# Performance work log

Hardware: AMD Instinct MI355X
Metric: run time of the kernel (lower is better)

The kernel has to match this reference:

```python
import jax, jax.numpy as jnp
import numpy as np
from jax import lax

# dims
B, T_MEL, N_MEL, L_TXT, D_TXT = 8, 400, 80, 128, 512
E, HID, EMB, N_SPK = 256, 256, 128, 100
H = HID // 2  # per-direction LSTM hidden


def setup_inputs() -> dict:
    key = jax.random.key(0)
    ks = jax.random.split(key, 16)
    def n(k, shape, s=0.02):
        return jax.random.normal(k, shape, jnp.float32) * s
    return {
        "x": n(ks[0], (B, N_MEL, T_MEL), 1.0),
        "input_lengths": jax.random.randint(ks[1], (B,), T_MEL // 2, T_MEL + 1).astype(jnp.int32),
        "text": n(ks[2], (B, L_TXT, D_TXT), 1.0),
        "text_lengths": jax.random.randint(ks[3], (B,), L_TXT // 2, L_TXT + 1).astype(jnp.int32),
        "Wx": n(ks[4], (E, N_MEL)), "bx": jnp.zeros((E,), jnp.float32),
        "Wq": n(ks[5], (E, D_TXT)), "bq": jnp.zeros((E,), jnp.float32),
        "Wout": n(ks[6], (E, E)), "bout": jnp.zeros((E,), jnp.float32),
        "v": jax.random.normal(ks[7], (E, 1), jnp.float32) * 0.1,
        "lstm_wih": n(ks[8], (2, 2, 4 * H, HID)),
        "lstm_whh": n(ks[9], (2, 2, 4 * H, H)),
        "lstm_bih": jnp.zeros((2, 2, 4 * H), jnp.float32),
        "lstm_bhh": jnp.zeros((2, 2, 4 * H), jnp.float32),
        "p1_w": n(ks[10], (EMB, HID)), "p1_b": jnp.zeros((EMB,), jnp.float32),
        "p2_w": n(ks[11], (N_SPK, EMB)), "p2_b": jnp.zeros((N_SPK,), jnp.float32),
    }


def _run_lstm(x, Wih, Whh, bih, bhh):
    # x: [B, L, in] -> outputs [B, L, H]; PyTorch gate order i,f,g,o
    h0 = jnp.zeros((x.shape[0], Whh.shape[1]), x.dtype)
    c0 = jnp.zeros_like(h0)
    def step(carry, xt):
        h, c = carry
        g = xt @ Wih.T + h @ Whh.T + (bih + bhh)
        i, f, gg, o = jnp.split(g, 4, axis=-1)
        c = jax.nn.sigmoid(f) * c + jax.nn.sigmoid(i) * jnp.tanh(gg)
        h = jax.nn.sigmoid(o) * jnp.tanh(c)
        return (h, c), h
    _, hs = lax.scan(step, (h0, c0), x.swapaxes(0, 1))  # scan over time
    return hs.swapaxes(0, 1)


def _reverse_by_length(x, lengths):
    # reverse the first lengths[b] steps of each sequence (pack_padded semantics)
    L = x.shape[1]
    idx = jnp.clip(lengths[:, None] - 1 - jnp.arange(L)[None, :], 0, L - 1)
    return jnp.take_along_axis(x, idx[:, :, None], axis=1)


def reference(x, input_lengths, text, text_lengths, Wx, bx, Wq, bq, Wout, bout, v,
              lstm_wih, lstm_whh, lstm_bih, lstm_bhh, p1_w, p1_b, p2_w, p2_b):
    # ---- vectorized VanillaAttention over all text tokens ----
    mels = x.swapaxes(1, 2)                       # [B, T, M]
    x1 = mels @ Wx.T + bx                         # [B, T, E]   linear_x
    q1 = text @ Wq.T + bq                         # [B, L, E]   linear_q
    # v^T @ out_linear(tanh(.)) == tanh(.) @ (Wout^T v) + v . bout
    w = Wout.T @ v[:, 0]                          # [E]
    c = bout @ v[:, 0]                            # scalar
    s = jnp.tanh(x1[:, None, :, :] + q1[:, :, None, :])   # [B, L, T, E]
    scores = jnp.einsum('blte,e->blt', s, w) + c           # [B, L, T]
    mel_mask = jnp.arange(T_MEL)[None, :] < input_lengths[:, None]   # [B, T]
    scores = jnp.where(mel_mask[:, None, :], scores, -jnp.inf)
    scores = jax.nn.softmax(scores, axis=-1)
    contexts = jnp.einsum('blt,bte->ble', scores, x1)       # [B, L, E]
    h = q1 + contexts                                       # LSTM input

    # ---- 2-layer bidirectional LSTM (packed semantics via per-length reversal) ----
    for layer in range(2):
        fwd = _run_lstm(h, lstm_wih[layer, 0], lstm_whh[layer, 0], lstm_bih[layer, 0], lstm_bhh[layer, 0])
        rev = _reverse_by_length(h, text_lengths)
        bwd = _run_lstm(rev, lstm_wih[layer, 1], lstm_whh[layer, 1], lstm_bih[layer, 1], lstm_bhh[layer, 1])
        bwd = _reverse_by_length(bwd, text_lengths)
        h = jnp.concatenate([fwd, bwd], axis=-1)            # [B, L, HID]

    # ---- masked mean pool (pad_packed zeros the padding before the sum) ----
    txt_mask = (jnp.arange(L_TXT)[None, :] < text_lengths[:, None]).astype(h.dtype)
    pooled = (h * txt_mask[:, :, None]).sum(axis=1) / text_lengths[:, None].astype(h.dtype)

    out = jnp.tanh(pooled @ p1_w.T + p1_b)
    embeddings = out / jnp.linalg.norm(out, axis=1, keepdims=True)
    logits = out @ p2_w.T + p2_b
    return logits, embeddings, scores
```

## Files before the change

kernel.cpp:

```cpp
#include <hip/hip_runtime.h>
#include <hip/hip_bf16.h>
#include <math.h>

#define B 8
#define T_MEL 400
#define N_MEL 80
#define L_TXT 128
#define D_TXT 512
#define E 256
#define HID 256
#define EMB 128
#define N_SPK 100
#define HH 128

#define OFF_W      0
#define OFF_C      256
#define OFF_WXT    272
#define OFF_WQT    (OFF_WXT + N_MEL*E)
#define OFF_WIHT   (OFF_WQT + D_TXT*E)
#define OFF_BSUM   (OFF_WIHT + 2*2*256*512)
#define OFF_X1     (OFF_BSUM + 2048)
#define OFF_Q1     (OFF_X1 + B*T_MEL*E)
#define OFF_G      OFF_X1
#define OFF_H0     (OFF_Q1 + B*L_TXT*E)
#define OFF_O1     (OFF_H0 + B*L_TXT*E)
#define OFF_HS0    OFF_H0
#define OFF_HS1    OFF_O1

typedef _Float16 half2v __attribute__((ext_vector_type(2)));

__device__ __forceinline__ float fast_sigmoid(float x){ return 1.f/(1.f+__expf(-x)); }
__device__ __forceinline__ float fast_tanh(float x){ float e=__expf(2.f*x); return 1.f - 2.f/(e+1.f); }

__device__ __forceinline__ float fdot2(uint a, uint b, float c){
  half2v ha = __builtin_bit_cast(half2v, a);
  half2v hb = __builtin_bit_cast(half2v, b);
#if __has_builtin(__builtin_amdgcn_fdot2)
  return __builtin_amdgcn_fdot2(ha, hb, c, false);
#else
  float r;
  asm("v_dot2_f32_f16 %0, %1, %2, %3" : "=v"(r) : "v"(a), "v"(b), "v"(c));
  return r;
#endif
}
__device__ __forceinline__ uint packh2(float a, float b){
  union { _Float16 h[2]; uint u; } x;
  x.h[0] = (_Float16)a; x.h[1] = (_Float16)b; return x.u;
}

__global__ __launch_bounds__(256) void k_prep(const float* __restrict__ Wout, const float* __restrict__ bout,
                       const float* __restrict__ v,    const float* __restrict__ Wx,
                       const float* __restrict__ Wq,   const float* __restrict__ wih,
                       const float* __restrict__ bih,  const float* __restrict__ bhh,
                       float* __restrict__ ws){
  int blk = blockIdx.x, tid = threadIdx.x;
  if (blk == 0){
    float acc = 0.f;
    for (int j=0;j<E;j++) acc += Wout[j*E + tid] * v[j];
    ws[OFF_W + tid] = acc;
    if (tid==0){ float c=0.f; for(int j=0;j<E;j++) c += bout[j]*v[j]; ws[OFF_C]=c; }
  } else if (blk <= N_MEL){
    int m = blk-1;
    ws[OFF_WXT + m*E + tid] = Wx[tid*N_MEL + m];
  } else if (blk <= N_MEL + D_TXT){
    int k = blk-1-N_MEL;
    ws[OFF_WQT + k*E + tid] = Wq[tid*D_TXT + k];
  } else if (blk <= N_MEL + D_TXT + 512){
    int idx = blk-1-N_MEL-D_TXT;
    int ld = idx >> 7, k2 = idx & 127;
    uint* wout = (uint*)(ws + OFF_WIHT) + (size_t)idx*512;
    for (int g = tid; g < 512; g += 256){
      float a = wih[((size_t)(ld*512+g))*256 + 2*k2];
      float b = wih[((size_t)(ld*512+g))*256 + 2*k2 + 1];
      wout[g] = packh2(a, b);
    }
  } else {
    for (int i = tid; i < 2048; i += 256)
      ws[OFF_BSUM + i] = bih[i] + bhh[i];
  }
}

__global__ __launch_bounds__(256) void k_xq(const float* __restrict__ x,    const float* __restrict__ bx,
                                            const float* __restrict__ text, const float* __restrict__ bq,
                                            float* __restrict__ ws){
  __shared__ float sbuf[2048];
  int blk = blockIdx.x, tid = threadIdx.x;
  if (blk < 800){
    int b = blk/100; int t0 = (blk%100)*4;
    float (*sx)[4] = (float(*)[4])sbuf;
    for (int i = tid; i < N_MEL*4; i += 256){
      int m = i>>2, ii = i&3;
      sx[m][ii] = x[(b*N_MEL+m)*T_MEL + t0 + ii];
    }
    __syncthreads();
    float bxe = bx[tid];
    float a0=bxe,a1=bxe,a2=bxe,a3=bxe;
    const float* wxt = ws + OFF_WXT;
    #pragma unroll 4
    for (int m=0;m<N_MEL;m++){
      float w = wxt[m*E + tid];
      a0 += sx[m][0]*w; a1 += sx[m][1]*w; a2 += sx[m][2]*w; a3 += sx[m][3]*w;
    }
    float* x1 = ws + OFF_X1 + (b*T_MEL + t0)*E + tid;
    x1[0]=a0; x1[E]=a1; x1[2*E]=a2; x1[3*E]=a3;
  } else {
    int bb = blk - 800;
    int b = bb/32; int l0 = (bb%32)*4;
    float (*st)[D_TXT] = (float(*)[D_TXT])sbuf;
    for (int i = tid; i < 4*D_TXT; i += 256){
      int li = i / D_TXT, k = i % D_TXT;
      st[li][k] = text[(b*L_TXT + l0 + li)*D_TXT + k];
    }
    __syncthreads();
    float bqe = bq[tid];
    float a0=bqe,a1=bqe,a2=bqe,a3=bqe;
    const float* wqt = ws + OFF_WQT;
    #pragma unroll 2
    for (int k=0;k<D_TXT;k++){
      float w = wqt[k*E + tid];
      a0 += st[0][k]*w; a1 += st[1][k]*w; a2 += st[2][k]*w; a3 += st[3][k]*w;
    }
    float* q1 = ws + OFF_Q1 + (b*L_TXT + l0)*E + tid;
    q1[0]=a0; q1[E]=a1; q1[2*E]=a2; q1[3*E]=a3;
  }
}

__global__ __launch_bounds__(256) void k_score(const int* __restrict__ mel_len,
                                               float* __restrict__ ws,
                                               float* __restrict__ d_out){
  int blk = blockIdx.x; int b = blk >> 7; int l = blk & 127;
  int tid = threadIdx.x; int lane = tid & 63; int wv = tid >> 6;
  __shared__ __align__(16) float sl[T_MEL];
  __shared__ float red[8];
  const float* x1 = ws + OFF_X1 + b*T_MEL*E;
  const float* q1 = ws + OFF_Q1 + (b*L_TXT+l)*E;
  int g = lane >> 4, i = lane & 15;
  float qv[16], wvv[16];
  {
    const float4* q4 = (const float4*)(q1 + i*16);
    const float4* w4 = (const float4*)(ws + OFF_W + i*16);
    #pragma unroll
    for (int j=0;j<4;j++){
      float4 a = q4[j]; qv[4*j]=a.x; qv[4*j+1]=a.y; qv[4*j+2]=a.z; qv[4*j+3]=a.w;
      float4 c = w4[j]; wvv[4*j]=c.x; wvv[4*j+1]=c.y; wvv[4*j+2]=c.z; wvv[4*j+3]=c.w;
    }
  }
  float cc = ws[OFF_C];
  int len = mel_len[b];
  #pragma unroll 2
  for (int iter=0; iter<25; iter++){
    int t = iter*16 + wv*4 + g;
    const float4* xr = (const float4*)(x1 + t*E + i*16);
    float s = 0.f;
    #pragma unroll
    for (int j=0;j<4;j++){
      float4 xv = xr[j];
      s += wvv[4*j+0]*fast_tanh(xv.x + qv[4*j+0]);
      s += wvv[4*j+1]*fast_tanh(xv.y + qv[4*j+1]);
      s += wvv[4*j+2]*fast_tanh(xv.z + qv[4*j+2]);
      s += wvv[4*j+3]*fast_tanh(xv.w + qv[4*j+3]);
    }
    s += __shfl_xor(s,1); s += __shfl_xor(s,2);
    s += __shfl_xor(s,4); s += __shfl_xor(s,8);
    if (i==0) sl[t] = s + cc;
  }
  __syncthreads();
  float mx = -3.0e38f;
  for (int t = tid; t < T_MEL; t += 256) if (t < len) mx = fmaxf(mx, sl[t]);
  #pragma unroll
  for (int off=32; off>=1; off>>=1) mx = fmaxf(mx, __shfl_xor(mx, off));
  if (lane==0) red[wv] = mx;
  __syncthreads();
  mx = fmaxf(fmaxf(red[0],red[1]),fmaxf(red[2],red[3]));
  float se = 0.f;
  for (int t = tid; t < T_MEL; t += 256){
    float p = (t < len) ? __expf(sl[t]-mx) : 0.f;
    sl[t] = p; se += p;
  }
  #pragma unroll
  for (int off=32; off>=1; off>>=1) se += __shfl_xor(se, off);
  if (lane==0) red[4+wv] = se;
  __syncthreads();
  float rsum = 1.f/(red[4]+red[5]+red[6]+red[7]);
  float* sc_out = d_out + 1824 + (b*L_TXT + l)*T_MEL;
  for (int t = tid; t < T_MEL; t += 256){
    float p = sl[t]*rsum;
    sl[t] = p; sc_out[t] = p;
  }
  __syncthreads();
  float a = 0.f;
  int e = tid;
  for (int t = 0; t < T_MEL; t += 4){
    float4 p4 = *(const float4*)&sl[t];
    a += p4.x*x1[(t  )*E+e] + p4.y*x1[(t+1)*E+e]
       + p4.z*x1[(t+2)*E+e] + p4.w*x1[(t+3)*E+e];
  }
  ws[OFF_H0 + (b*L_TXT+l)*E + e] = q1[e] + a;
}

__global__ __launch_bounds__(512) void k_gates(const float* __restrict__ in,
                                               const float* __restrict__ hs,
                                               const int* __restrict__ txt_len,
                                               float* __restrict__ gates, int layer,
                                               float* __restrict__ ws){
  int idx = blockIdx.x; int tt = idx & 15; int dir = (idx>>4)&1; int b = idx>>5;
  int tid = threadIdx.x;
  __shared__ __align__(16) uint sih[8][128];
  int len = txt_len[b];
  for (int i = tid; i < 8*128; i += 512){
    int r = i >> 7, k2 = i & 127;
    int t = tt*8 + r;
    int row = dir ? max(0, len-1-t) : t;
    float va, vb;
    if (layer == 0){
      const float2 p = *(const float2*)&in[((size_t)(b*L_TXT + row))*HID + 2*k2];
      va = p.x; vb = p.y;
    } else {
      int k = 2*k2; int d = k >> 7, u = k & 127;
      int sidx = (d==0) ? row : (row < len ? len-1-row : 0);
      const float* hr = hs + (((size_t)(d*8+b)*128) + u)*128 + sidx;
      va = hr[0]; vb = hr[128];
    }
    sih[r][k2] = packh2(va, vb);
  }
  __syncthreads();
  int ld = layer*2 + dir;
  int g = tid;
  float bsum = ws[OFF_BSUM + ld*512 + g];
  float acc[8];
  #pragma unroll
  for (int r=0;r<8;r++) acc[r] = bsum;
  const uint* wt2 = (const uint*)(ws + OFF_WIHT) + (size_t)ld*128*512 + g;
  for (int k4=0; k4<128; k4+=4){
    uint w0 = wt2[(k4  )*512];
    uint w1 = wt2[(k4+1)*512];
    uint w2 = wt2[(k4+2)*512];
    uint w3 = wt2[(k4+3)*512];
    #pragma unroll
    for (int r=0;r<8;r++){
      uint4 s4 = *(const uint4*)&sih[r][k4];
      acc[r] = fdot2(s4.x, w0, acc[r]);
      acc[r] = fdot2(s4.y, w1, acc[r]);
      acc[r] = fdot2(s4.z, w2, acc[r]);
      acc[r] = fdot2(s4.w, w3, acc[r]);
    }
  }
  float* go = gates + (((size_t)(dir*L_TXT + tt*8)*8) + b)*512 + g;
  #pragma unroll
  for (int r=0;r<8;r++) go[(size_t)r*8*512] = acc[r];
}

__global__ __launch_bounds__(512) void k_scan(const float* __restrict__ Gp,
                                              const float* __restrict__ whh_all,
                                              float* __restrict__ hseq, int layer){
  int dir = blockIdx.x & 1; int b = blockIdx.x >> 1;
  int tid = threadIdx.x;
  int l = tid & 63, w = tid >> 6;
  int gt = l >> 4;
  int li = l & 15;
  int u  = w*16 + li;
  int row = gt*128 + u;

  __shared__ uint wlds[32768];
  __shared__ uint h2buf[2][64];

  const float* wr = whh_all + ((size_t)((layer*2+dir)*512 + row))*HH;
  #pragma unroll
  for (int j=0;j<16;j++){
    uint4 vv;
    vv.x = packh2(wr[j*8+0], wr[j*8+1]);
    vv.y = packh2(wr[j*8+2], wr[j*8+3]);
    vv.z = packh2(wr[j*8+4], wr[j*8+5]);
    vv.w = packh2(wr[j*8+6], wr[j*8+7]);
    *(uint4*)(wlds + w*4096 + j*256 + l*4) = vv;
  }
  if (tid < 128) ((uint*)h2buf)[tid] = 0;

  const float* gb = Gp + ((size_t)(dir*L_TXT)*8 + b)*512 + row;
  float gi = gb[0];
  float c_reg = 0.f;
  float hm1=0.f, hm2=0.f, hm3=0.f;
  bool isg = (gt==2);
  __syncthreads();

  const uint4* wp = (const uint4*)(wlds + w*4096 + l*4);
  float* hout = hseq + (((size_t)(dir*8+b)*128) + u)*128;

  for (int s=0; s<L_TXT; s++){
    float gnext = gb[(size_t)(s+1 < L_TXT ? s+1 : s)*4096];
    const uint4* hp = (const uint4*)(h2buf[s&1]);
    float p0 = gi, p1 = 0.f, p2 = 0.f, p3 = 0.f;
    #pragma unroll
    for (int j=0;j<16;j+=4){
      uint4 A0 = wp[(j  )*64], H0 = hp[j  ];
      uint4 A1 = wp[(j+1)*64], H1 = hp[j+1];
      uint4 A2 = wp[(j+2)*64], H2 = hp[j+2];
      uint4 A3 = wp[(j+3)*64], H3 = hp[j+3];
      p0 = fdot2(A0.x,H0.x,p0); p0 = fdot2(A0.y,H0.y,p0);
      p0 = fdot2(A0.z,H0.z,p0); p0 = fdot2(A0.w,H0.w,p0);
      p1 = fdot2(A1.x,H1.x,p1); p1 = fdot2(A1.y,H1.y,p1);
      p1 = fdot2(A1.z,H1.z,p1); p1 = fdot2(A1.w,H1.w,p1);
      p2 = fdot2(A2.x,H2.x,p2); p2 = fdot2(A2.y,H2.y,p2);
      p2 = fdot2(A2.z,H2.z,p2); p2 = fdot2(A2.w,H2.w,p2);
      p3 = fdot2(A3.x,H3.x,p3); p3 = fdot2(A3.y,H3.y,p3);
      p3 = fdot2(A3.z,H3.z,p3); p3 = fdot2(A3.w,H3.w,p3);
    }
    float acc = (p0+p1)+(p2+p3);
    float xa = isg ? 2.f*acc : acc;
    float sg = 1.f/(1.f+__expf(-xa));
    float val = isg ? 2.f*sg - 1.f : sg;
    float x  = __shfl_xor(val, 16);
    float y0 = __shfl_xor(val, 32);
    float y1 = __shfl_xor(x,   32);
    float iv = (gt==0)?val : (gt==1)?x  : (gt==2)?y0 : y1;
    float fv = (gt==0)?x   : (gt==1)?val: (gt==2)?y1 : y0;
    float gv = (gt==0)?y0  : (gt==1)?y1 : (gt==2)?val: x;
    float ov = (gt==0)?y1  : (gt==1)?y0 : (gt==2)?x  : val;
    c_reg = fv*c_reg + iv*gv;
    float h = ov*fast_tanh(c_reg);
    float hn = __shfl_xor(h, 1);
    if (gt==0 && !(li&1)) h2buf[(s+1)&1][u>>1] = packh2(h, hn);
    if (gt==0 && (s&3)==3)
      *(float4*)&hout[s-3] = make_float4(hm3, hm2, hm1, h);
    hm3 = hm2; hm2 = hm1; hm1 = h;
    gi = gnext;
    __syncthreads();
  }
}

__global__ __launch_bounds__(256) void k_final(const float* __restrict__ hs,
                                               const int* __restrict__ txt_len,
                                               const float* __restrict__ p1w,
                                               const float* __restrict__ p1b,
                                               const float* __restrict__ p2w,
                                               const float* __restrict__ p2b,
                                               float* __restrict__ d_out){
  int b = blockIdx.x; int tid = threadIdx.x;
  __shared__ float pl[HID];
  __shared__ float ol[EMB];
  __shared__ float nrm;
  int len = txt_len[b];
  int d = tid >> 7, u = tid & 127;
  const float* hrow = hs + (((size_t)(d*8+b)*128) + u)*128;
  float s = 0.f;
  int t4 = len & ~3;
  for (int t=0; t<t4; t+=4){
    float4 p = *(const float4*)&hrow[t];
    s += (p.x + p.y) + (p.z + p.w);
  }
  for (int t=t4; t<len; t++) s += hrow[t];
  pl[tid] = s / (float)len;
  __syncthreads();
  if (tid < EMB){
    float a = p1b[tid];
    for (int k=0;k<HID;k++) a += pl[k]*p1w[tid*HID+k];
    ol[tid] = fast_tanh(a);
  }
  __syncthreads();
  if (tid == 0){
    float q = 0.f;
    for (int k=0;k<EMB;k++) q += ol[k]*ol[k];
    nrm = rsqrtf(q);
  }
  __syncthreads();
  if (tid < EMB) d_out[800 + b*EMB + tid] = ol[tid]*nrm;
  if (tid < N_SPK){
    float a = p2b[tid];
    for (int k=0;k<EMB;k++) a += ol[k]*p2w[tid*EMB+k];
    d_out[b*N_SPK + tid] = a;
  }
}

extern "C" void kernel_launch(void* const* d_in, const int* in_sizes, int n_in,
                              void* d_out, int out_size, void* d_ws, size_t ws_size,
                              hipStream_t stream) {
  const float* x       = (const float*)d_in[0];
  const int*   mel_len = (const int*)  d_in[1];
  const float* text    = (const float*)d_in[2];
  const int*   txt_len = (const int*)  d_in[3];
  const float* Wx      = (const float*)d_in[4];
  const float* bx      = (const float*)d_in[5];
  const float* Wq      = (const float*)d_in[6];
  const float* bq      = (const float*)d_in[7];
  const float* Wout    = (const float*)d_in[8];
  const float* bout    = (const float*)d_in[9];
  const float* v       = (const float*)d_in[10];
  const float* wih     = (const float*)d_in[11];
  const float* whh     = (const float*)d_in[12];
  const float* bih     = (const float*)d_in[13];
  const float* bhh     = (const float*)d_in[14];
  const float* p1w     = (const float*)d_in[15];
  const float* p1b     = (const float*)d_in[16];
  const float* p2w     = (const float*)d_in[17];
  const float* p2b     = (const float*)d_in[18];
  float* ws  = (float*)d_ws;
  float* out = (float*)d_out;

  k_prep <<<1106, 256, 0, stream>>>(Wout, bout, v, Wx, Wq, wih, bih, bhh, ws);
  k_xq   <<<1056, 256, 0, stream>>>(x, bx, text, bq, ws);
  k_score<<<1024, 256, 0, stream>>>(mel_len, ws, out);

  float* G = ws + OFF_G;
  k_gates<<<256, 512, 0, stream>>>(ws + OFF_H0, ws + OFF_HS0, txt_len, G, 0, ws);
  k_scan <<<16, 512, 0, stream>>>(G, whh, ws + OFF_HS0, 0);
  k_gates<<<256, 512, 0, stream>>>(ws + OFF_H0, ws + OFF_HS0, txt_len, G, 1, ws);
  k_scan <<<16, 512, 0, stream>>>(G, whh, ws + OFF_HS1, 1);

  k_final<<<8, 256, 0, stream>>>(ws + OFF_HS1, txt_len, p1w, p1b, p2w, p2b, out);
}
```

Baseline: 461.0 us.

## Restructure LSTM scan to compute all four gates per thread pair and fuse pooling

The recurrent scan kernel drops from 512 to 256 threads per block. Each pair of threads now splits the hidden-dimension dot product for all four gates of one unit and combines the halves with a shuffle, replacing the old scheme of one gate per thread with cross-lane gate exchange. In layer 1 the scan accumulates the masked sum for mean pooling directly instead of writing the hidden sequence, so the final kernel reads pooled sums rather than re-reading the full sequence. The aim is less per-step shuffle and select overhead and less sequence traffic, at the cost of more dot-product work per thread on the serial critical path.

```diff
diff --git a/kernel.cpp b/kernel.cpp
--- a/kernel.cpp
+++ b/kernel.cpp
@@ -25,7 +25,7 @@
 #define OFF_H0     (OFF_Q1 + B*L_TXT*E)
 #define OFF_O1     (OFF_H0 + B*L_TXT*E)
 #define OFF_HS0    OFF_H0
-#define OFF_HS1    OFF_O1
+#define OFF_POOL   OFF_O1
 
 typedef _Float16 half2v __attribute__((ext_vector_type(2)));
 
@@ -250,85 +250,97 @@
   for (int r=0;r<8;r++) go[(size_t)r*8*512] = acc[r];
 }
 
-__global__ __launch_bounds__(512) void k_scan(const float* __restrict__ Gp,
+__global__ __launch_bounds__(256) void k_scan(const float* __restrict__ Gp,
                                               const float* __restrict__ whh_all,
-                                              float* __restrict__ hseq, int layer){
+                                              const int* __restrict__ txt_len,
+                                              float* __restrict__ hseq,
+                                              float* __restrict__ pooled, int layer){
   int dir = blockIdx.x & 1; int b = blockIdx.x >> 1;
   int tid = threadIdx.x;
   int l = tid & 63, w = tid >> 6;
-  int gt = l >> 4;
-  int li = l & 15;
-  int u  = w*16 + li;
-  int row = gt*128 + u;
+  int u  = tid >> 1;
+  int hf = tid & 1;
 
   __shared__ uint wlds[32768];
   __shared__ uint h2buf[2][64];
 
-  const float* wr = whh_all + ((size_t)((layer*2+dir)*512 + row))*HH;
+  const float* wbase = whh_all + (size_t)(layer*2+dir)*512*HH;
   #pragma unroll
-  for (int j=0;j<16;j++){
-    uint4 vv;
-    vv.x = packh2(wr[j*8+0], wr[j*8+1]);
-    vv.y = packh2(wr[j*8+2], wr[j*8+3]);
-    vv.z = packh2(wr[j*8+4], wr[j*8+5]);
-    vv.w = packh2(wr[j*8+6], wr[j*8+7]);
-    *(uint4*)(wlds + w*4096 + j*256 + l*4) = vv;
+  for (int r=0;r<4;r++){
+    const float* wr = wbase + (size_t)(r*128+u)*HH + 64*hf;
+    #pragma unroll
+    for (int jj=0;jj<8;jj++){
+      uint4 vv;
+      vv.x = packh2(wr[jj*8+0], wr[jj*8+1]);
+      vv.y = packh2(wr[jj*8+2], wr[jj*8+3]);
+      vv.z = packh2(wr[jj*8+4], wr[jj*8+5]);
+      vv.w = packh2(wr[jj*8+6], wr[jj*8+7]);
+      *(uint4*)(wlds + w*8192 + (r*8+jj)*256 + l*4) = vv;
+    }
   }
   if (tid < 128) ((uint*)h2buf)[tid] = 0;
-
-  const float* gb = Gp + ((size_t)(dir*L_TXT)*8 + b)*512 + row;
-  float gi = gb[0];
-  float c_reg = 0.f;
+  int len = txt_len[b];
+  bool pool = (layer == 1);
+
+  const float* gb = Gp + ((size_t)(dir*L_TXT)*8 + b)*512 + u;
+  float g0 = gb[0], g1 = gb[128], g2 = gb[256], g3 = gb[384];
+  float c_reg = 0.f, psum = 0.f;
   float hm1=0.f, hm2=0.f, hm3=0.f;
-  bool isg = (gt==2);
-  __syncthreads();
-
-  const uint4* wp = (const uint4*)(wlds + w*4096 + l*4);
+  __syncthreads();
+
+  const uint4* wp = (const uint4*)(wlds + w*8192 + l*4);
   float* hout = hseq + (((size_t)(dir*8+b)*128) + u)*128;
 
   for (int s=0; s<L_TXT; s++){
-    float gnext = gb[(size_t)(s+1 < L_TXT ? s+1 : s)*4096];
-    const uint4* hp = (const uint4*)(h2buf[s&1]);
-    float p0 = gi, p1 = 0.f, p2 = 0.f, p3 = 0.f;
+    const float* gn = gb + (size_t)(s+1 < L_TXT ? s+1 : s)*4096;
+    float n0 = gn[0], n1 = gn[128], n2 = gn[256], n3 = gn[384];
+    const uint4* hp = (const uint4*)(h2buf[s&1] + hf*32);
+    float a0 = hf ? 0.f : g0;
+    float a1 = hf ? 0.f : g1;
+    float a2 = hf ? 0.f : g2;
+    float a3 = hf ? 0.f : g3;
     #pragma unroll
-    for (int j=0;j<16;j+=4){
-      uint4 A0 = wp[(j  )*64], H0 = hp[j  ];
-      uint4 A1 = wp[(j+1)*64], H1 = hp[j+1];
-      uint4 A2 = wp[(j+2)*64], H2 = hp[j+2];
-      uint4 A3 = wp[(j+3)*64], H3 = hp[j+3];
-      p0 = fdot2(A0.x,H0.x,p0); p0 = fdot2(A0.y,H0.y,p0);
-      p0 = fdot2(A0.z,H0.z,p0); p0 = fdot2(A0.w,H0.w,p0);
-      p1 = fdot2(A1.x,H1.x,p1); p1 = fdot2(A1.y,H1.y,p1);
-      p1 = fdot2(A1.z,H1.z,p1); p1 = fdot2(A1.w,H1.w,p1);
-      p2 = fdot2(A2.x,H2.x,p2); p2 = fdot2(A2.y,H2.y,p2);
-      p2 = fdot2(A2.z,H2.z,p2); p2 = fdot2(A2.w,H2.w,p2);
-      p3 = fdot2(A3.x,H3.x,p3); p3 = fdot2(A3.y,H3.y,p3);
-      p3 = fdot2(A3.z,H3.z,p3); p3 = fdot2(A3.w,H3.w,p3);
-    }
-    float acc = (p0+p1)+(p2+p3);
-    float xa = isg ? 2.f*acc : acc;
-    float sg = 1.f/(1.f+__expf(-xa));
-    float val = isg ? 2.f*sg - 1.f : sg;
-    float x  = __shfl_xor(val, 16);
-    float y0 = __shfl_xor(val, 32);
-    float y1 = __shfl_xor(x,   32);
-    float iv = (gt==0)?val : (gt==1)?x  : (gt==2)?y0 : y1;
-    float fv = (gt==0)?x   : (gt==1)?val: (gt==2)?y1 : y0;
-    float gv = (gt==0)?y0  : (gt==1)?y1 : (gt==2)?val: x;
-    float ov = (gt==0)?y1  : (gt==1)?y0 : (gt==2)?x  : val;
-    c_reg = fv*c_reg + iv*gv;
-    float h = ov*fast_tanh(c_reg);
-    float hn = __shfl_xor(h, 1);
-    if (gt==0 && !(li&1)) h2buf[(s+1)&1][u>>1] = packh2(h, hn);
-    if (gt==0 && (s&3)==3)
-      *(float4*)&hout[s-3] = make_float4(hm3, hm2, hm1, h);
-    hm3 = hm2; hm2 = hm1; hm1 = h;
-    gi = gnext;
+    for (int jj=0;jj<8;jj++){
+      uint4 hv = hp[jj];
+      uint4 w0 = wp[(jj   )*64];
+      uint4 w1 = wp[( 8+jj)*64];
+      uint4 w2 = wp[(16+jj)*64];
+      uint4 w3 = wp[(24+jj)*64];
+      a0 = fdot2(w0.x,hv.x,a0); a0 = fdot2(w0.y,hv.y,a0);
+      a0 = fdot2(w0.z,hv.z,a0); a0 = fdot2(w0.w,hv.w,a0);
+      a1 = fdot2(w1.x,hv.x,a1); a1 = fdot2(w1.y,hv.y,a1);
+      a1 = fdot2(w1.z,hv.z,a1); a1 = fdot2(w1.w,hv.w,a1);
+      a2 = fdot2(w2.x,hv.x,a2); a2 = fdot2(w2.y,hv.y,a2);
+      a2 = fdot2(w2.z,hv.z,a2); a2 = fdot2(w2.w,hv.w,a2);
+      a3 = fdot2(w3.x,hv.x,a3); a3 = fdot2(w3.y,hv.y,a3);
+      a3 = fdot2(w3.z,hv.z,a3); a3 = fdot2(w3.w,hv.w,a3);
+    }
+    a0 += __shfl_xor(a0, 1);
+    a1 += __shfl_xor(a1, 1);
+    a2 += __shfl_xor(a2, 1);
+    a3 += __shfl_xor(a3, 1);
+    float i_ = fast_sigmoid(a0);
+    float f_ = fast_sigmoid(a1);
+    float g_ = fast_tanh   (a2);
+    float o_ = fast_sigmoid(a3);
+    c_reg = f_*c_reg + i_*g_;
+    float h = o_*fast_tanh(c_reg);
+    float hn = __shfl_xor(h, 2);
+    if (hf==0 && !(u&1)) h2buf[(s+1)&1][u>>1] = packh2(h, hn);
+    if (pool){
+      if (s < len) psum += h;
+    } else {
+      if (hf==0 && (s&3)==3)
+        *(float4*)&hout[s-3] = make_float4(hm3, hm2, hm1, h);
+      hm3 = hm2; hm2 = hm1; hm1 = h;
+    }
+    g0 = n0; g1 = n1; g2 = n2; g3 = n3;
     __syncthreads();
   }
-}
-
-__global__ __launch_bounds__(256) void k_final(const float* __restrict__ hs,
+  if (pool && hf==0) pooled[((size_t)(dir*8+b))*128 + u] = psum;
+}
+
+__global__ __launch_bounds__(256) void k_final(const float* __restrict__ pooled,
                                                const int* __restrict__ txt_len,
                                                const float* __restrict__ p1w,
                                                const float* __restrict__ p1b,
@@ -341,15 +353,7 @@
   __shared__ float nrm;
   int len = txt_len[b];
   int d = tid >> 7, u = tid & 127;
-  const float* hrow = hs + (((size_t)(d*8+b)*128) + u)*128;
-  float s = 0.f;
-  int t4 = len & ~3;
-  for (int t=0; t<t4; t+=4){
-    float4 p = *(const float4*)&hrow[t];
-    s += (p.x + p.y) + (p.z + p.w);
-  }
-  for (int t=t4; t<len; t++) s += hrow[t];
-  pl[tid] = s / (float)len;
+  pl[tid] = pooled[((size_t)(d*8+b))*128 + u] / (float)len;
   __syncthreads();
   if (tid < EMB){
     float a = p1b[tid];
@@ -402,9 +406,9 @@
 
   float* G = ws + OFF_G;
   k_gates<<<256, 512, 0, stream>>>(ws + OFF_H0, ws + OFF_HS0, txt_len, G, 0, ws);
-  k_scan <<<16, 512, 0, stream>>>(G, whh, ws + OFF_HS0, 0);
+  k_scan <<<16, 256, 0, stream>>>(G, whh, txt_len, ws + OFF_HS0, ws + OFF_POOL, 0);
   k_gates<<<256, 512, 0, stream>>>(ws + OFF_H0, ws + OFF_HS0, txt_len, G, 1, ws);
-  k_scan <<<16, 512, 0, stream>>>(G, whh, ws + OFF_HS1, 1);
-
-  k_final<<<8, 256, 0, stream>>>(ws + OFF_HS1, txt_len, p1w, p1b, p2w, p2b, out);
-}
+  k_scan <<<16, 256, 0, stream>>>(G, whh, txt_len, ws + OFF_HS0, ws + OFF_POOL, 1);
+
+  k_final<<<8, 256, 0, stream>>>(ws + OFF_POOL, txt_len, p1w, p1b, p2w, p2b, out);
+}
```

Result: no change. 453.5 us (-1.6%).
